# Kernel optimization log

Measured on AMD Instinct MI355X. Metric: run time of the kernel, lower is better.

Reference implementation:

```python
import jax, jax.numpy as jnp
import numpy as np
from jax import lax
from jax.scipy.special import logsumexp

EPS = 0.01 ** 2      # blur^p, geomloss SamplesLoss(p=2, blur=0.01)
N_ITERS = 20         # fixed Sinkhorn iterations (log-domain)


def setup_inputs() -> dict:
    key = jax.random.key(0)
    k1, k2 = jax.random.split(key)
    p_q = jax.random.normal(k1, (4, 4096, 3), dtype=jnp.float32)
    p_gt = jax.random.normal(k2, (4, 4096, 4), dtype=jnp.float32)
    return {"p_q": p_q, "p_gt": p_gt}


def _cost(x, y):
    # C_ij = 0.5 * ||x_i - y_j||^2   (geomloss p=2 convention), [B,N,M]
    x2 = jnp.sum(x * x, -1)
    y2 = jnp.sum(y * y, -1)
    xy = jnp.einsum('bnd,bmd->bnm', x, y)
    return 0.5 * (x2[:, :, None] + y2[:, None, :] - 2.0 * xy)


def _softmin(C, pot, logw, axis):
    # -eps * logsumexp over `axis` of (pot - C)/eps + logw ; pot/logw broadcast on `axis`'s dual
    if axis == 2:
        z = (pot[:, None, :] - C) / EPS + logw  # reduce over M -> [B,N]
    else:
        z = (pot[:, :, None] - C) / EPS + logw  # reduce over N -> [B,M]
    return -EPS * logsumexp(z, axis=axis)


def _ot_potentials(C, loga, logb):
    # asymmetric log-domain Sinkhorn; iterate on detached cost (envelope theorem,
    # matching geomloss' detach-then-extrapolate gradient), final differentiable step.
    Cd = lax.stop_gradient(C)
    B, N, M = C.shape

    def body(i, fg):
        f, g = fg
        f = _softmin(Cd, g, logb, axis=2)
        g = _softmin(Cd, f, loga, axis=1)
        return (f, g)

    f0 = jnp.zeros((B, N), C.dtype)
    g0 = jnp.zeros((B, M), C.dtype)
    f, g = lax.fori_loop(0, N_ITERS, body, (f0, g0))
    fd, gd = lax.stop_gradient(f), lax.stop_gradient(g)
    f = _softmin(C, gd, logb, axis=2)
    g = _softmin(C, fd, loga, axis=1)
    return f, g


def _sym_potential(C, logw):
    # symmetric Sinkhorn for OT(a,a): single potential, damped updates
    Cd = lax.stop_gradient(C)
    B, N, _ = C.shape

    def body(i, f):
        return 0.5 * (f + _softmin(Cd, f, logw, axis=2))

    f = lax.fori_loop(0, N_ITERS, body, jnp.zeros((B, N), C.dtype))
    return _softmin(C, lax.stop_gradient(f), logw, axis=2)


def reference(p_q, p_gt):
    x = p_q                 # [B,N,3]
    y = p_gt[:, :, :3]      # [B,M,3]
    B, N, _ = x.shape
    M = y.shape[1]
    loga = jnp.full((1, 1), -jnp.log(N), x.dtype)  # uniform weights (broadcast)
    logb = jnp.full((1, 1), -jnp.log(M), x.dtype)

    Cxy = _cost(x, y)
    Cxx = _cost(x, x)
    Cyy = _cost(y, y)

    f_ab, g_ab = _ot_potentials(Cxy, loga[:, :, None] * 0 - jnp.log(N), logb)
    # note: loga used in softmin over N-axis needs [.., :, None] broadcast; build explicitly:
    loga_b = jnp.full((B, N, 1), -jnp.log(N), x.dtype)
    logb_b = jnp.full((B, 1, M), -jnp.log(M), x.dtype)
    f_ab = _softmin(Cxy, lax.stop_gradient(g_ab), logb_b, axis=2)  # idempotent re-extrapolation
    g_ab = _softmin(Cxy, lax.stop_gradient(f_ab), loga_b, axis=1)
    f_aa = _sym_potential(Cxx, jnp.full((B, 1, N), -jnp.log(N), x.dtype))
    g_bb = _sym_potential(Cyy, logb_b)

    # debiased Sinkhorn divergence per batch: <a, f_ab - f_aa> + <b, g_ab - g_bb>
    L = jnp.mean(f_ab - f_aa, axis=1) + jnp.mean(g_ab - g_bb, axis=1)
    return L
```

## Files before the change

### kernel.cpp

```cpp
#include <hip/hip_runtime.h>
#include <math.h>

#define NPTS 4096
#define NBATCH 4
#define BLOCK 512
#define RPW 8

static constexpr float KSCALE     = 1.4426950408889634f / 1e-4f;
static constexpr float INVK2      = 1.0f / (KSCALE * KSCALE);
static constexpr float EPSLN2     = 1e-4f * 0.6931471805599453f;
static constexpr float NEGEPSLOGW = 8.31776616671934e-4f;
static constexpr float THR        = 20.0f;

__device__ __forceinline__ float fexp2(float x){
#if __has_builtin(__builtin_amdgcn_exp2f)
  return __builtin_amdgcn_exp2f(x);
#else
  return exp2f(x);
#endif
}
__device__ __forceinline__ float flog2(float x){
#if __has_builtin(__builtin_amdgcn_logf)
  return __builtin_amdgcn_logf(x);
#else
  return log2f(x);
#endif
}
__device__ __forceinline__ float frl(float x){
  return __int_as_float(__builtin_amdgcn_readfirstlane(__float_as_int(x)));
}

__global__ __launch_bounds__(BLOCK, 4) void softmin_kernel(
    const float* __restrict__ rowA, int rsA, const float4* __restrict__ pkInA,
    float4* __restrict__ pkOutA, const float* __restrict__ hOldA,
    float* __restrict__ outA, int modeA,
    const float* __restrict__ rowB, int rsB, const float4* __restrict__ pkInB,
    float4* __restrict__ pkOutB, const float* __restrict__ hOldB,
    float* __restrict__ outB, int modeB)
{
  __shared__ float4 qs[NPTS];

  int bid = blockIdx.x;
  const float* rowp; const float4* pkin; float4* pkout; const float* hold;
  float* outp; int rs, mode;
  if (bid < 256) { rowp=rowA; pkin=pkInA; pkout=pkOutA; hold=hOldA; outp=outA; rs=rsA; mode=modeA; }
  else           { rowp=rowB; pkin=pkInB; pkout=pkOutB; hold=hOldB; outp=outB; rs=rsB; mode=modeB; }
  int lb = bid & 255;
  int b  = lb >> 6;
  int rb = lb & 63;

  int tid = threadIdx.x;
  int lane = tid & 63;
  int wu = __builtin_amdgcn_readfirstlane(tid >> 6);
  int r0 = rb*64 + wu*RPW;
  int ridx0 = b*NPTS + r0;

  {
    const float4* src = pkin + b*NPTS;
    #pragma unroll
    for (int i = 0; i < NPTS/BLOCK; ++i)
      qs[i*BLOCK + tid] = src[i*BLOCK + tid];
  }

  float sx[RPW], sy[RPW], sz[RPW], hh[RPW];
  #pragma unroll
  for (int i = 0; i < RPW; ++i) {
    const float* p = rowp + (size_t)(ridx0 + i) * rs;
    sx[i] = frl(p[0]*KSCALE); sy[i] = frl(p[1]*KSCALE); sz[i] = frl(p[2]*KSCALE);
    hh[i] = frl(hold[ridx0 + i]);
  }

  __syncthreads();

  if (bid < 256) {
    float cmax[4][RPW];
    #pragma unroll
    for (int c = 0; c < 4; ++c)
      #pragma unroll
      for (int r = 0; r < RPW; ++r) cmax[c][r] = -INFINITY;

    #pragma unroll
    for (int c = 0; c < 4; ++c) {
      #pragma unroll
      for (int g = 0; g < 4; ++g) {
        int base = c*1024 + g*256 + lane;
        float4 q0 = qs[base], q1 = qs[base+64], q2 = qs[base+128], q3 = qs[base+192];
        #pragma unroll
        for (int r = 0; r < RPW; ++r) {
          float t0 = fmaf(sx[r],q0.x,fmaf(sy[r],q0.y,fmaf(sz[r],q0.z,q0.w)));
          float t1 = fmaf(sx[r],q1.x,fmaf(sy[r],q1.y,fmaf(sz[r],q1.z,q1.w)));
          float t2 = fmaf(sx[r],q2.x,fmaf(sy[r],q2.y,fmaf(sz[r],q2.z,q2.w)));
          float t3 = fmaf(sx[r],q3.x,fmaf(sy[r],q3.y,fmaf(sz[r],q3.z,q3.w)));
          float u  = fmaxf(fmaxf(t0,t1),t2);
          cmax[c][r] = fmaxf(fmaxf(u,t3),cmax[c][r]);
        }
      }
    }

    float M[RPW];
    #pragma unroll
    for (int r = 0; r < RPW; ++r) {
      float mm = fmaxf(fmaxf(cmax[0][r],cmax[1][r]), fmaxf(cmax[2][r],cmax[3][r]));
      #pragma unroll
      for (int off = 32; off; off >>= 1) mm = fmaxf(mm, __shfl_xor(mm, off, 64));
      M[r] = mm;
    }

    float S[RPW];
    #pragma unroll
    for (int r = 0; r < RPW; ++r) S[r] = 0.f;

    #pragma unroll
    for (int c = 0; c < 4; ++c) {
      int am = 0;
      #pragma unroll
      for (int r = 0; r < RPW; ++r)
        am |= __any(cmax[c][r] > M[r] - THR) ? (1 << r) : 0;
      if (am) {
        #pragma unroll
        for (int g = 0; g < 4; ++g) {
          int base = c*1024 + g*256 + lane;
          float4 q0 = qs[base], q1 = qs[base+64], q2 = qs[base+128], q3 = qs[base+192];
          #pragma unroll
          for (int r = 0; r < RPW; ++r) if (am & (1 << r)) {
            float t0 = fmaf(sx[r],q0.x,fmaf(sy[r],q0.y,fmaf(sz[r],q0.z,q0.w)));
            float t1 = fmaf(sx[r],q1.x,fmaf(sy[r],q1.y,fmaf(sz[r],q1.z,q1.w)));
            float t2 = fmaf(sx[r],q2.x,fmaf(sy[r],q2.y,fmaf(sz[r],q2.z,q2.w)));
            float t3 = fmaf(sx[r],q3.x,fmaf(sy[r],q3.y,fmaf(sz[r],q3.z,q3.w)));
            float u  = fmaxf(fmaxf(t0,t1),t2);
            float v  = fmaxf(u,t3);
            if (__any(v > M[r] - THR)) {
              float e0 = fexp2(t0-M[r]) + fexp2(t1-M[r]);
              float e1 = fexp2(t2-M[r]) + fexp2(t3-M[r]);
              S[r] += e0 + e1;
            }
          }
        }
      }
    }

    #pragma unroll
    for (int r = 0; r < RPW; ++r) {
      float s = S[r];
      #pragma unroll
      for (int off = 32; off; off >>= 1) s += __shfl_xor(s, off, 64);
      float ch = 0.5f*(sx[r]*sx[r] + sy[r]*sy[r] + sz[r]*sz[r]) * INVK2;
      float res = fmaf(-EPSLN2, M[r] + flog2(s), ch + NEGEPSLOGW);
      if (lane == r) {
        if (mode) res = 0.5f*(hh[r] + res);
        outp[ridx0 + r] = res;
        ((float*)(pkout + (ridx0 + r)))[3] = (res - ch) * KSCALE;
      }
    }
  } else {
    float M[RPW], S[RPW], chv[RPW];
    #pragma unroll
    for (int r = 0; r < RPW; ++r) {
      chv[r] = 0.5f*(sx[r]*sx[r] + sy[r]*sy[r] + sz[r]*sz[r]) * INVK2;
      M[r] = (hh[r] + chv[r]) * KSCALE;
      S[r] = 0.f;
    }

    #pragma unroll
    for (int g = 0; g < 16; ++g) {
      int base = g*256 + lane;
      float4 q0 = qs[base], q1 = qs[base+64], q2 = qs[base+128], q3 = qs[base+192];
      #pragma unroll
      for (int r = 0; r < RPW; ++r) {
        float t0 = fmaf(sx[r],q0.x,fmaf(sy[r],q0.y,fmaf(sz[r],q0.z,q0.w)));
        float t1 = fmaf(sx[r],q1.x,fmaf(sy[r],q1.y,fmaf(sz[r],q1.z,q1.w)));
        float t2 = fmaf(sx[r],q2.x,fmaf(sy[r],q2.y,fmaf(sz[r],q2.z,q2.w)));
        float t3 = fmaf(sx[r],q3.x,fmaf(sy[r],q3.y,fmaf(sz[r],q3.z,q3.w)));
        float u    = fmaxf(fmaxf(t0,t1),t2);
        float cmax = fmaxf(u,t3);
        if (__any(cmax > M[r] - THR)) {
          float Mn = fmaxf(M[r], cmax);
          float sc = fexp2(M[r] - Mn);
          float e0 = fexp2(t0-Mn) + fexp2(t1-Mn);
          float e1 = fexp2(t2-Mn) + fexp2(t3-Mn);
          S[r] = fmaf(S[r], sc, e0 + e1);
          M[r] = Mn;
        }
      }
    }

    #pragma unroll
    for (int r = 0; r < RPW; ++r) {
      float mm = M[r];
      #pragma unroll
      for (int off = 32; off; off >>= 1) mm = fmaxf(mm, __shfl_xor(mm, off, 64));
      float s = S[r] * fexp2(M[r] - mm);
      #pragma unroll
      for (int off = 32; off; off >>= 1) s += __shfl_xor(s, off, 64);
      float res = fmaf(-EPSLN2, mm + flog2(s), chv[r] + NEGEPSLOGW);
      if (lane == r) {
        if (mode) res = 0.5f*(hh[r] + res);
        outp[ridx0 + r] = res;
        ((float*)(pkout + (ridx0 + r)))[3] = (res - chv[r]) * KSCALE;
      }
    }
  }
}

__global__ void pack_init(const float* __restrict__ x, const float* __restrict__ y,
                          float4* pkfab, float4* pkgab,
                          float4* pkfaa0, float4* pkfaa1,
                          float4* pkgbb0, float4* pkgbb1)
{
  int i = blockIdx.x*256 + threadIdx.x;
  const float* xp = x + (size_t)i*3;
  float xx = xp[0], xy = xp[1], xz = xp[2];
  float4 vx; vx.x=xx; vx.y=xy; vx.z=xz;
  vx.w = -0.5f*(xx*xx + xy*xy + xz*xz)*KSCALE;
  const float* yp = y + (size_t)i*4;
  float yx = yp[0], yy = yp[1], yz = yp[2];
  float4 vy; vy.x=yx; vy.y=yy; vy.z=yz;
  vy.w = -0.5f*(yx*yx + yy*yy + yz*yz)*KSCALE;
  pkgab[i]  = vx; pkfaa0[i] = vx; pkfaa1[i] = vx;
  pkfab[i]  = vy; pkgbb0[i] = vy; pkgbb1[i] = vy;
}

__global__ void reduce_kernel(const float* __restrict__ fab, const float* __restrict__ faa,
                              const float* __restrict__ gab, const float* __restrict__ gbb,
                              float* __restrict__ out)
{
  int b = blockIdx.x;
  int tid = threadIdx.x;
  float s = 0.f;
  for (int i = tid; i < NPTS; i += 256) {
    int idx = b*NPTS + i;
    s += (fab[idx] - faa[idx]) + (gab[idx] - gbb[idx]);
  }
  for (int off = 32; off > 0; off >>= 1) s += __shfl_down(s, off, 64);
  __shared__ float red[4];
  if ((tid & 63) == 0) red[tid >> 6] = s;
  __syncthreads();
  if (tid == 0) out[b] = (red[0]+red[1]+red[2]+red[3]) * (1.0f/NPTS);
}

extern "C" void kernel_launch(void* const* d_in, const int* in_sizes, int n_in,
                              void* d_out, int out_size, void* d_ws, size_t ws_size,
                              hipStream_t stream)
{
  const float* x = (const float*)d_in[0];
  const float* y = (const float*)d_in[1];
  float* ws = (float*)d_ws;
  const size_t P = (size_t)NBATCH * NPTS;

  float* f_ab    = ws + 0*P;
  float* g_ab    = ws + 1*P;
  float* faaR[2] = { ws + 2*P, ws + 4*P };
  float* gbbR[2] = { ws + 3*P, ws + 5*P };
  float4* pk4    = (float4*)(ws + 6*P);
  float4* PKfab    = pk4 + 0*P;
  float4* PKgab    = pk4 + 1*P;
  float4* PKfaa[2] = { pk4 + 2*P, pk4 + 3*P };
  float4* PKgbb[2] = { pk4 + 4*P, pk4 + 5*P };

  hipMemsetAsync(ws + 2*P, 0, 2*P*sizeof(float), stream);
  pack_init<<<dim3(P/256), dim3(256), 0, stream>>>(x, y, PKfab, PKgab,
                                                   PKfaa[0], PKfaa[1], PKgbb[0], PKgbb[1]);

  for (int i = 0; i < 21; ++i) {
    int cur = i & 1, nxt = cur ^ 1;
    int modeS = (i < 20) ? 1 : 0;
    softmin_kernel<<<512, BLOCK, 0, stream>>>(
        x, 3, PKfab, PKgab, f_ab, f_ab, 0,
        x, 3, PKfaa[cur], PKfaa[nxt], faaR[cur], faaR[nxt], modeS);
    softmin_kernel<<<512, BLOCK, 0, stream>>>(
        y, 4, PKgab, PKfab, g_ab, g_ab, 0,
        y, 4, PKgbb[cur], PKgbb[nxt], gbbR[cur], gbbR[nxt], modeS);
  }
  reduce_kernel<<<dim3(4), dim3(256), 0, stream>>>(f_ab, faaR[1], g_ab, gbbR[1], (float*)d_out);
}
```

Measured before the change: 910.7 us.

## Single-pass online softmin for cross-OT seeded with previous iteration's argmax column

The asymmetric (xy) softmin blocks previously did two passes over all columns: one to find the row max, then a second pass that computed exponentials only for chunks within a threshold of the max. They now do one online-logsumexp pass. Each row's running max is seeded from the argmax column stored by the previous iteration, so most groups fail the threshold test and their exponentials are skipped. This removes the separate max pass but adds argmax tracking, rescaling exponentials, and a per-row int buffer that is read and written every launch.

```diff
diff --git a/kernel.cpp b/kernel.cpp
--- a/kernel.cpp
+++ b/kernel.cpp
@@ -33,7 +33,7 @@
 __global__ __launch_bounds__(BLOCK, 4) void softmin_kernel(
     const float* __restrict__ rowA, int rsA, const float4* __restrict__ pkInA,
     float4* __restrict__ pkOutA, const float* __restrict__ hOldA,
-    float* __restrict__ outA, int modeA,
+    float* __restrict__ outA, int modeA, int* __restrict__ jmaxA,
     const float* __restrict__ rowB, int rsB, const float4* __restrict__ pkInB,
     float4* __restrict__ pkOutB, const float* __restrict__ hOldB,
     float* __restrict__ outB, int modeB)
@@ -63,93 +63,76 @@
   }
 
   float sx[RPW], sy[RPW], sz[RPW], hh[RPW];
+  int jp[RPW];
   #pragma unroll
   for (int i = 0; i < RPW; ++i) {
     const float* p = rowp + (size_t)(ridx0 + i) * rs;
     sx[i] = frl(p[0]*KSCALE); sy[i] = frl(p[1]*KSCALE); sz[i] = frl(p[2]*KSCALE);
     hh[i] = frl(hold[ridx0 + i]);
+    jp[i] = (bid < 256) ? __builtin_amdgcn_readfirstlane(jmaxA[ridx0 + i]) : 0;
   }
 
   __syncthreads();
 
   if (bid < 256) {
-    float cmax[4][RPW];
-    #pragma unroll
-    for (int c = 0; c < 4; ++c)
-      #pragma unroll
-      for (int r = 0; r < RPW; ++r) cmax[c][r] = -INFINITY;
-
-    #pragma unroll
-    for (int c = 0; c < 4; ++c) {
-      #pragma unroll
-      for (int g = 0; g < 4; ++g) {
-        int base = c*1024 + g*256 + lane;
-        float4 q0 = qs[base], q1 = qs[base+64], q2 = qs[base+128], q3 = qs[base+192];
-        #pragma unroll
-        for (int r = 0; r < RPW; ++r) {
-          float t0 = fmaf(sx[r],q0.x,fmaf(sy[r],q0.y,fmaf(sz[r],q0.z,q0.w)));
-          float t1 = fmaf(sx[r],q1.x,fmaf(sy[r],q1.y,fmaf(sz[r],q1.z,q1.w)));
-          float t2 = fmaf(sx[r],q2.x,fmaf(sy[r],q2.y,fmaf(sz[r],q2.z,q2.w)));
-          float t3 = fmaf(sx[r],q3.x,fmaf(sy[r],q3.y,fmaf(sz[r],q3.z,q3.w)));
-          float u  = fmaxf(fmaxf(t0,t1),t2);
-          cmax[c][r] = fmaxf(fmaxf(u,t3),cmax[c][r]);
+    float M[RPW], S[RPW];
+    int   jb[RPW];
+    #pragma unroll
+    for (int r = 0; r < RPW; ++r) {
+      float4 qd = qs[jp[r]];
+      M[r] = fmaf(sx[r],qd.x,fmaf(sy[r],qd.y,fmaf(sz[r],qd.z,qd.w)));
+      S[r] = 0.f;
+      jb[r] = jp[r];
+    }
+
+    #pragma unroll
+    for (int g = 0; g < 16; ++g) {
+      int base = g*256 + lane;
+      float4 q0 = qs[base], q1 = qs[base+64], q2 = qs[base+128], q3 = qs[base+192];
+      #pragma unroll
+      for (int r = 0; r < RPW; ++r) {
+        float t0 = fmaf(sx[r],q0.x,fmaf(sy[r],q0.y,fmaf(sz[r],q0.z,q0.w)));
+        float t1 = fmaf(sx[r],q1.x,fmaf(sy[r],q1.y,fmaf(sz[r],q1.z,q1.w)));
+        float t2 = fmaf(sx[r],q2.x,fmaf(sy[r],q2.y,fmaf(sz[r],q2.z,q2.w)));
+        float t3 = fmaf(sx[r],q3.x,fmaf(sy[r],q3.y,fmaf(sz[r],q3.z,q3.w)));
+        float a01 = fmaxf(t0,t1);
+        float a23 = fmaxf(t2,t3);
+        float cmax = fmaxf(a01,a23);
+        if (__any(cmax > M[r] - THR)) {
+          int j01 = t1 > t0  ? base+64  : base;
+          int j23 = t3 > t2  ? base+192 : base+128;
+          int jg  = a23 > a01 ? j23 : j01;
+          jb[r] = (cmax > M[r]) ? jg : jb[r];
+          float Mn = fmaxf(M[r], cmax);
+          float sc = fexp2(M[r] - Mn);
+          float e0 = fexp2(t0-Mn) + fexp2(t1-Mn);
+          float e1 = fexp2(t2-Mn) + fexp2(t3-Mn);
+          S[r] = fmaf(S[r], sc, e0 + e1);
+          M[r] = Mn;
         }
       }
     }
 
-    float M[RPW];
-    #pragma unroll
-    for (int r = 0; r < RPW; ++r) {
-      float mm = fmaxf(fmaxf(cmax[0][r],cmax[1][r]), fmaxf(cmax[2][r],cmax[3][r]));
-      #pragma unroll
-      for (int off = 32; off; off >>= 1) mm = fmaxf(mm, __shfl_xor(mm, off, 64));
-      M[r] = mm;
-    }
-
-    float S[RPW];
-    #pragma unroll
-    for (int r = 0; r < RPW; ++r) S[r] = 0.f;
-
-    #pragma unroll
-    for (int c = 0; c < 4; ++c) {
-      int am = 0;
-      #pragma unroll
-      for (int r = 0; r < RPW; ++r)
-        am |= __any(cmax[c][r] > M[r] - THR) ? (1 << r) : 0;
-      if (am) {
-        #pragma unroll
-        for (int g = 0; g < 4; ++g) {
-          int base = c*1024 + g*256 + lane;
-          float4 q0 = qs[base], q1 = qs[base+64], q2 = qs[base+128], q3 = qs[base+192];
-          #pragma unroll
-          for (int r = 0; r < RPW; ++r) if (am & (1 << r)) {
-            float t0 = fmaf(sx[r],q0.x,fmaf(sy[r],q0.y,fmaf(sz[r],q0.z,q0.w)));
-            float t1 = fmaf(sx[r],q1.x,fmaf(sy[r],q1.y,fmaf(sz[r],q1.z,q1.w)));
-            float t2 = fmaf(sx[r],q2.x,fmaf(sy[r],q2.y,fmaf(sz[r],q2.z,q2.w)));
-            float t3 = fmaf(sx[r],q3.x,fmaf(sy[r],q3.y,fmaf(sz[r],q3.z,q3.w)));
-            float u  = fmaxf(fmaxf(t0,t1),t2);
-            float v  = fmaxf(u,t3);
-            if (__any(v > M[r] - THR)) {
-              float e0 = fexp2(t0-M[r]) + fexp2(t1-M[r]);
-              float e1 = fexp2(t2-M[r]) + fexp2(t3-M[r]);
-              S[r] += e0 + e1;
-            }
-          }
-        }
-      }
-    }
-
-    #pragma unroll
-    for (int r = 0; r < RPW; ++r) {
-      float s = S[r];
+    #pragma unroll
+    for (int r = 0; r < RPW; ++r) {
+      float mm = M[r]; int jj = jb[r];
+      #pragma unroll
+      for (int off = 32; off; off >>= 1) {
+        float mo = __shfl_xor(mm, off, 64);
+        int   jo = __shfl_xor(jj, off, 64);
+        jj = (mo > mm) ? jo : jj;
+        mm = fmaxf(mo, mm);
+      }
+      float s = S[r] * fexp2(M[r] - mm);
       #pragma unroll
       for (int off = 32; off; off >>= 1) s += __shfl_xor(s, off, 64);
       float ch = 0.5f*(sx[r]*sx[r] + sy[r]*sy[r] + sz[r]*sz[r]) * INVK2;
-      float res = fmaf(-EPSLN2, M[r] + flog2(s), ch + NEGEPSLOGW);
+      float res = fmaf(-EPSLN2, mm + flog2(s), ch + NEGEPSLOGW);
       if (lane == r) {
         if (mode) res = 0.5f*(hh[r] + res);
         outp[ridx0 + r] = res;
         ((float*)(pkout + (ridx0 + r)))[3] = (res - ch) * KSCALE;
+        jmaxA[ridx0 + r] = jj;
       }
     }
   } else {
@@ -205,7 +188,8 @@
 __global__ void pack_init(const float* __restrict__ x, const float* __restrict__ y,
                           float4* pkfab, float4* pkgab,
                           float4* pkfaa0, float4* pkfaa1,
-                          float4* pkgbb0, float4* pkgbb1)
+                          float4* pkgbb0, float4* pkgbb1,
+                          int* jmaxFab, int* jmaxGab)
 {
   int i = blockIdx.x*256 + threadIdx.x;
   const float* xp = x + (size_t)i*3;
@@ -218,6 +202,7 @@
   vy.w = -0.5f*(yx*yx + yy*yy + yz*yz)*KSCALE;
   pkgab[i]  = vx; pkfaa0[i] = vx; pkfaa1[i] = vx;
   pkfab[i]  = vy; pkgbb0[i] = vy; pkgbb1[i] = vy;
+  jmaxFab[i] = 0; jmaxGab[i] = 0;
 }
 
 __global__ void reduce_kernel(const float* __restrict__ fab, const float* __restrict__ faa,
@@ -251,7 +236,9 @@
   float* g_ab    = ws + 1*P;
   float* faaR[2] = { ws + 2*P, ws + 4*P };
   float* gbbR[2] = { ws + 3*P, ws + 5*P };
-  float4* pk4    = (float4*)(ws + 6*P);
+  int*   jmaxFab = (int*)(ws + 6*P);
+  int*   jmaxGab = (int*)(ws + 7*P);
+  float4* pk4    = (float4*)(ws + 8*P);
   float4* PKfab    = pk4 + 0*P;
   float4* PKgab    = pk4 + 1*P;
   float4* PKfaa[2] = { pk4 + 2*P, pk4 + 3*P };
@@ -259,16 +246,17 @@
 
   hipMemsetAsync(ws + 2*P, 0, 2*P*sizeof(float), stream);
   pack_init<<<dim3(P/256), dim3(256), 0, stream>>>(x, y, PKfab, PKgab,
-                                                   PKfaa[0], PKfaa[1], PKgbb[0], PKgbb[1]);
+                                                   PKfaa[0], PKfaa[1], PKgbb[0], PKgbb[1],
+                                                   jmaxFab, jmaxGab);
 
   for (int i = 0; i < 21; ++i) {
     int cur = i & 1, nxt = cur ^ 1;
     int modeS = (i < 20) ? 1 : 0;
     softmin_kernel<<<512, BLOCK, 0, stream>>>(
-        x, 3, PKfab, PKgab, f_ab, f_ab, 0,
+        x, 3, PKfab, PKgab, f_ab, f_ab, 0, jmaxFab,
         x, 3, PKfaa[cur], PKfaa[nxt], faaR[cur], faaR[nxt], modeS);
     softmin_kernel<<<512, BLOCK, 0, stream>>>(
-        y, 4, PKgab, PKfab, g_ab, g_ab, 0,
+        y, 4, PKgab, PKfab, g_ab, g_ab, 0, jmaxGab,
         y, 4, PKgbb[cur], PKgbb[nxt], gbbR[cur], gbbR[nxt], modeS);
   }
   reduce_kernel<<<dim3(4), dim3(256), 0, stream>>>(f_ab, faaR[1], g_ab, gbbR[1], (float*)d_out);
```

New measurement: 939.2 us. 1.03x slower.
